# Performance work log

Measured on AMD Instinct MI355X. Metric: run time of the kernel, lower is better.

The kernel has to match this reference:

```python
import jax, jax.numpy as jnp
import numpy as np


def position_encoding(feature_size, d_model):
    pos = jnp.arange(feature_size, dtype=jnp.float32)[:, None]
    _2i = jnp.arange(0, d_model, 2, dtype=jnp.float32)
    ang = pos / jnp.power(10000.0, _2i / d_model)  # [F, D/2]
    pe = jnp.zeros((feature_size, d_model), dtype=jnp.float32)
    pe = pe.at[:, 0::2].set(jnp.sin(ang))
    pe = pe.at[:, 1::2].set(jnp.cos(ang))
    return pe


def setup_inputs() -> dict:
    key = jax.random.key(0)
    ks = jax.random.split(key, 11)
    B, F, D, T, V = 32, 512, 256, 32, 128
    sc = 0.02
    return {
        "f": jax.random.normal(ks[0], (B, F, D), dtype=jnp.float32),
        "decoder_input_ids": jax.random.randint(ks[1], (B, T), 0, V),
        "emb": sc * jax.random.normal(ks[2], (V, D), dtype=jnp.float32),
        "w_e": sc * jax.random.normal(ks[3], (D, D), dtype=jnp.float32),
        "w_h": sc * jax.random.normal(ks[4], (D, D), dtype=jnp.float32),
        "w_f": sc * jax.random.normal(ks[5], (D, D), dtype=jnp.float32),
        "w_q": sc * jax.random.normal(ks[6], (D, D), dtype=jnp.float32),
        "w_s": sc * jax.random.normal(ks[7], (D, D), dtype=jnp.float32),
        "w_g": sc * jax.random.normal(ks[8], (D, 2 * D), dtype=jnp.float32),
        "w_ih": sc * jax.random.normal(ks[9], (4 * D, 2 * D), dtype=jnp.float32),
        "w_hh": sc * jax.random.normal(ks[10], (4 * D, D), dtype=jnp.float32),
    }


def reference(f, decoder_input_ids, emb, w_e, w_h, w_f, w_q, w_s, w_g, w_ih, w_hh):
    B, F, D = f.shape
    q = position_encoding(F, D)                      # [F, D]
    dec = emb[decoder_input_ids]                     # [B, T, D]
    # loop-invariant attention terms, hoisted: w_f(f) + w_q(q)
    base = jnp.einsum('bfd,od->bfo', f, w_f) + (q @ w_q.T)[None]  # [B, F, D]
    fq = f + q[None]                                 # [B, F, D]

    def step(carry, x_t):
        h, cell, s, cp = carry
        # LSTMCell (bias=False), torch gate order i, f, g, o
        xin = jnp.concatenate([x_t, cp], axis=-1)    # [B, 2D]
        gates = xin @ w_ih.T + h @ w_hh.T            # [B, 4D]
        gi, gf, gg, go = jnp.split(gates, 4, axis=-1)
        cell = jax.nn.sigmoid(gf) * cell + jax.nn.sigmoid(gi) * jnp.tanh(gg)
        h = jax.nn.sigmoid(go) * jnp.tanh(cell)
        # Bahdanau-style energy; softmax over feature (last) dim per source
        t_in = jnp.tanh((h @ w_h.T)[:, None] + base + jnp.einsum('bfd,od->bfo', s, w_s))
        e = jnp.einsum('bfd,od->bfo', t_in, w_e)     # [B, F, D]
        alpha = jax.nn.softmax(e, axis=-1)
        s = s + alpha
        c = (alpha * f).sum(1)                       # [B, D]
        cp = (alpha * fq).sum(1)                     # [B, D]
        pred = jnp.concatenate([c, h], axis=-1) @ w_g.T  # [B, D]
        return (h, cell, s, cp), pred

    z = jnp.zeros((B, D), dtype=f.dtype)
    carry0 = (z, z, jnp.zeros_like(f), z)
    _, preds = jax.lax.scan(step, carry0, jnp.swapaxes(dec, 0, 1))  # [T, B, D]
    return jnp.swapaxes(preds, 0, 1)                 # [B, T, D]
```

## Files before the change

kernel.cpp:

```cpp
#include <hip/hip_runtime.h>
#include <math.h>

#define NB 32
#define NF 512
#define ND 256
#define NT 32
#define RPB 32
#define NTILE (NF / RPB)
#define NBLK (NB * NTILE)
#define XS 260

typedef __attribute__((ext_vector_type(8))) short bf16x8;
typedef __attribute__((ext_vector_type(4))) short bf16x4;
typedef __attribute__((ext_vector_type(4))) float f32x4;

__device__ __forceinline__ float sigmoidf_(float x) { return 1.0f / (1.0f + __expf(-x)); }

__device__ __forceinline__ short f2bf(float x) {
    union { float f; unsigned u; } v; v.f = x;
    unsigned r = (v.u + 0x7FFF + ((v.u >> 16) & 1)) >> 16;
    return (short)r;
}

#define AGENT __HIP_MEMORY_SCOPE_AGENT
__device__ __forceinline__ float AL(const float* p) {
    return __hip_atomic_load(p, __ATOMIC_RELAXED, AGENT);
}
__device__ __forceinline__ void AS(float* p, float v) {
    __hip_atomic_store(p, v, __ATOMIC_RELAXED, AGENT);
}
__device__ __forceinline__ int APOLL(int* p) {
    return __hip_atomic_fetch_add(p, 0, __ATOMIC_RELAXED, AGENT);
}
__device__ __forceinline__ void SIGNAL(int* p, int tid, int coop) {
    asm volatile("s_waitcnt vmcnt(0)" ::: "memory");
    __syncthreads();
    if (coop && tid == 0) __hip_atomic_fetch_add(p, 1, __ATOMIC_RELAXED, AGENT);
}
__device__ __forceinline__ void WAITGE(int* p, int tgt, int tid) {
    if (tid == 0) {
        while (APOLL(p) < tgt) __builtin_amdgcn_s_sleep(2);
    }
    __syncthreads();
}

__global__ void pe_kernel(float* __restrict__ q) {
    int p = blockIdx.x;
    int d = threadIdx.x;
    float i2 = (float)((d >> 1) << 1);
    float rate = expf(-9.210340371976184f * (i2 / (float)ND));
    float ang = (float)p * rate;
    q[p * ND + d] = (d & 1) ? cosf(ang) : sinf(ang);
}

__global__ void wcvt_kernel(const float* __restrict__ w, short* __restrict__ wb, int n) {
    int i = blockIdx.x * 256 + threadIdx.x;
    if (i < n) wb[i] = f2bf(w[i]);
}

__global__ void wprep_kernel(const float* __restrict__ w_ih, const float* __restrict__ w_hh,
                             const float* __restrict__ w_h, const float* __restrict__ w_g,
                             float* __restrict__ wcat, float* __restrict__ w_hT,
                             float* __restrict__ w_gT) {
    int j = blockIdx.x;
    int o = threadIdx.x;
    wcat[(size_t)j * 768 + o]       = w_ih[(size_t)j * 512 + o];
    wcat[(size_t)j * 768 + 256 + o] = w_ih[(size_t)j * 512 + 256 + o];
    wcat[(size_t)j * 768 + 512 + o] = w_hh[(size_t)j * 256 + o];
    if (j < ND)  w_hT[(size_t)j * ND + o] = w_h[(size_t)o * ND + j];
    if (j < 512) w_gT[(size_t)j * ND + o] = w_g[(size_t)o * 512 + j];
}

__global__ void qwq_kernel(const float* __restrict__ q, const float* __restrict__ w_q,
                           float* __restrict__ qwq) {
    int p = blockIdx.x;
    int o = threadIdx.x;
    __shared__ float qs[ND];
    qs[o] = q[(size_t)p * ND + o];
    __syncthreads();
    const float4* wr = (const float4*)(w_q + (size_t)o * ND);
    float acc = 0.f;
    for (int k4 = 0; k4 < ND / 4; ++k4) {
        float4 w = wr[k4];
        int k = 4 * k4;
        acc += qs[k] * w.x + qs[k + 1] * w.y + qs[k + 2] * w.z + qs[k + 3] * w.w;
    }
    qwq[(size_t)p * ND + o] = acc;
}

__global__ void base_kernel(const float* __restrict__ fin, const float* __restrict__ w_f,
                            const float* __restrict__ qwq, float* __restrict__ bsum) {
    int b = blockIdx.x / NTILE;
    int f0 = (blockIdx.x % NTILE) * RPB;
    int o = threadIdx.x;
    __shared__ float fs[RPB][ND];
    #pragma unroll
    for (int r = 0; r < RPB; ++r)
        fs[r][o] = fin[((size_t)(b * NF + f0 + r)) * ND + o];
    __syncthreads();
    float acc[RPB];
    #pragma unroll
    for (int r = 0; r < RPB; ++r) acc[r] = 0.f;
    const float4* wr = (const float4*)(w_f + (size_t)o * ND);
    for (int k4 = 0; k4 < ND / 4; ++k4) {
        float4 w = wr[k4];
        int k = 4 * k4;
        #pragma unroll
        for (int r = 0; r < RPB; ++r)
            acc[r] += fs[r][k] * w.x + fs[r][k + 1] * w.y + fs[r][k + 2] * w.z + fs[r][k + 3] * w.w;
    }
    #pragma unroll
    for (int r = 0; r < RPB; ++r)
        bsum[((size_t)(b * NF + f0 + r)) * ND + o] = acc[r] + qwq[(size_t)(f0 + r) * ND + o];
}

__global__ void __launch_bounds__(256, 2) dec_persist(
        int coop, int t0, int smask,
        const float* __restrict__ fin, const int* __restrict__ ids,
        const float* __restrict__ emb, const float* __restrict__ qpe,
        float* __restrict__ bsum,
        const float* __restrict__ wcat, const float* __restrict__ w_hT,
        const float* __restrict__ w_gT,
        const short* __restrict__ w_e_bf, const short* __restrict__ w_s_bf,
        float* __restrict__ h, float* __restrict__ cell,
        float* __restrict__ gatesT,
        float* __restrict__ cpart, float* __restrict__ cppart,
        int* __restrict__ acount, int* __restrict__ gcount, int* __restrict__ hflag,
        float* __restrict__ out) {
    int bid = blockIdx.x;
    int tid = threadIdx.x;
    int l = tid & 63;
    int wv = tid >> 6;
    int c15 = l & 15;
    int g = l >> 4;
    int c = l;
    int b = bid >> 4;
    int tile = bid & 15;
    int f0 = tile * RPB;
    int o0 = wv * 64;

    __shared__ __align__(16) short tin_bf[RPB * ND];
    __shared__ float xfer[RPB * XS];
    __shared__ float cred[2][1024];
    __shared__ float sred[RPB][5];
    char* tb = (char*)tin_bf;
    float* zl = xfer;
    float* zp = xfer;
    float* hn = xfer;
    float* hwhl = xfer + 256;

    const size_t CP = (size_t)NTILE * NB * ND;

    int tbeg = coop ? 0 : t0;
    int tend = coop ? NT : t0;

    for (int t = tbeg; t <= tend; ++t) {
        int prd = (t > 0) ? ((t - 1) & 1) : 0;

        if ((smask & 1) && t < NT) {
            if (coop) {
                if (tid == 0) {
                    while (APOLL(&acount[b]) < 16 * t) __builtin_amdgcn_s_sleep(2);
                    while (APOLL(&hflag[b]) < t) __builtin_amdgcn_s_sleep(2);
                }
                __syncthreads();
            }
            float xv = emb[(size_t)ids[b * NT + t] * ND + tid];
            float cpsum = 0.f;
            if (t > 0) {
                #pragma unroll
                for (int tl = 0; tl < NTILE; ++tl)
                    cpsum += AL(&cppart[prd * CP + ((size_t)tl * NB + b) * ND + tid]);
            }
            zl[tid] = xv;
            zl[256 + tid] = cpsum;
            zl[512 + tid] = AL(&h[(size_t)(t & 1) * NB * ND + b * ND + tid]);
            __syncthreads();
            int j0 = tile * 64 + wv * 16;
            for (int jj = 0; jj < 16; ++jj) {
                int j = j0 + jj;
                const float* wr = wcat + (size_t)j * 768;
                float s = 0.f;
                #pragma unroll
                for (int i = 0; i < 12; ++i)
                    s += wr[l + i * 64] * zl[l + i * 64];
                #pragma unroll
                for (int off = 1; off <= 32; off <<= 1)
                    s += __shfl_xor(s, off);
                if (l == 0) AS(&gatesT[(size_t)b * 1024 + j], s);
            }
            SIGNAL(&gcount[b], tid, coop);
        }

        if ((smask & 2) && t < NT && tile == 0) {
            if (coop) WAITGE(&gcount[b], 16 * (t + 1), tid);
            float gi = AL(&gatesT[(size_t)b * 1024 + tid]);
            float gf = AL(&gatesT[(size_t)b * 1024 + 256 + tid]);
            float gg = AL(&gatesT[(size_t)b * 1024 + 512 + tid]);
            float go = AL(&gatesT[(size_t)b * 1024 + 768 + tid]);
            float cold = cell[(size_t)b * ND + tid];
            float cnew = sigmoidf_(gf) * cold + sigmoidf_(gi) * tanhf(gg);
            float hval = sigmoidf_(go) * tanhf(cnew);
            cell[(size_t)b * ND + tid] = cnew;
            AS(&h[(size_t)((t + 1) & 1) * NB * ND + b * ND + tid], hval);
            SIGNAL(&hflag[b], tid, coop);
        }

        if ((smask & 2) && t > 0 && tile == 1) {
            if (coop && t == NT) {
                if (tid == 0) {
                    while (APOLL(&acount[b]) < 16 * t) __builtin_amdgcn_s_sleep(2);
                    while (APOLL(&hflag[b]) < t) __builtin_amdgcn_s_sleep(2);
                }
                __syncthreads();
            }
            float csum = 0.f;
            #pragma unroll
            for (int tl = 0; tl < NTILE; ++tl)
                csum += AL(&cpart[prd * CP + ((size_t)tl * NB + b) * ND + tid]);
            zp[tid] = csum;
            zp[256 + tid] = AL(&h[(size_t)(t & 1) * NB * ND + b * ND + tid]);
            __syncthreads();
            float p = 0.f;
            #pragma unroll 8
            for (int k = 0; k < 512; ++k)
                p += zp[k] * w_gT[(size_t)k * ND + tid];
            out[((size_t)b * NT + (t - 1)) * ND + tid] = p;
            __syncthreads();
        }

        if (t >= NT) continue;

        if (smask & 4) {
            if (coop) WAITGE(&hflag[b], t + 1, tid);
            hn[tid] = AL(&h[(size_t)((t + 1) & 1) * NB * ND + b * ND + tid]);
            __syncthreads();
            {
                float a = 0.f;
                #pragma unroll 8
                for (int k = 0; k < ND; ++k)
                    a += hn[k] * w_hT[(size_t)k * ND + tid];
                hwhl[tid] = a;
            }
            __syncthreads();

            float4 bsv4[8];
            {
                float4 hwh4 = *(const float4*)&hwhl[4 * c];
                #pragma unroll
                for (int i = 0; i < 8; ++i) {
                    int r = wv + 4 * i;
                    bsv4[i] = *(const float4*)(bsum + ((size_t)(b * NF + f0 + r)) * ND + 4 * c);
                    bf16x4 tv;
                    tv.x = f2bf(tanhf(hwh4.x + bsv4[i].x));
                    tv.y = f2bf(tanhf(hwh4.y + bsv4[i].y));
                    tv.z = f2bf(tanhf(hwh4.z + bsv4[i].z));
                    tv.w = f2bf(tanhf(hwh4.w + bsv4[i].w));
                    *(bf16x4*)(tb + ((r * 512 + 8 * c) ^ ((r & 7) << 4))) = tv;
                }
            }
            __syncthreads();

            f32x4 acc[2][4];
            #pragma unroll
            for (int mt = 0; mt < 2; ++mt)
                #pragma unroll
                for (int nt = 0; nt < 4; ++nt)
                    acc[mt][nt] = (f32x4)0.f;
            #pragma unroll
            for (int ks = 0; ks < 8; ++ks) {
                int kb = ks * 32 + g * 8;
                bf16x8 afr[2];
                #pragma unroll
                for (int mt = 0; mt < 2; ++mt) {
                    int row = mt * 16 + c15;
                    afr[mt] = *(const bf16x8*)(tb + ((row * 512 + kb * 2) ^ ((row & 7) << 4)));
                }
                #pragma unroll
                for (int nt = 0; nt < 4; ++nt) {
                    int o = o0 + nt * 16 + c15;
                    bf16x8 bfr = *(const bf16x8*)(w_e_bf + (size_t)o * ND + kb);
                    #pragma unroll
                    for (int mt = 0; mt < 2; ++mt)
                        acc[mt][nt] = __builtin_amdgcn_mfma_f32_16x16x32_bf16(afr[mt], bfr, acc[mt][nt], 0, 0, 0);
                }
            }

            {
                float ps[2][4];
                #pragma unroll
                for (int mt = 0; mt < 2; ++mt)
                    #pragma unroll
                    for (int reg = 0; reg < 4; ++reg) ps[mt][reg] = 0.f;
                #pragma unroll
                for (int mt = 0; mt < 2; ++mt)
                    #pragma unroll
                    for (int nt = 0; nt < 4; ++nt)
                        #pragma unroll
                        for (int reg = 0; reg < 4; ++reg) {
                            float a = __expf(acc[mt][nt][reg]);
                            acc[mt][nt][reg] = a;
                            ps[mt][reg] += a;
                        }
                #pragma unroll
                for (int off = 1; off <= 8; off <<= 1)
                    #pragma unroll
                    for (int mt = 0; mt < 2; ++mt)
                        #pragma unroll
                        for (int reg = 0; reg < 4; ++reg)
                            ps[mt][reg] += __shfl_xor(ps[mt][reg], off);
                if (c15 == 0) {
                    #pragma unroll
                    for (int mt = 0; mt < 2; ++mt)
                        #pragma unroll
                        for (int reg = 0; reg < 4; ++reg)
                            sred[mt * 16 + g * 4 + reg][wv] = ps[mt][reg];
                }
                __syncthreads();
                #pragma unroll
                for (int mt = 0; mt < 2; ++mt)
                    #pragma unroll
                    for (int reg = 0; reg < 4; ++reg) {
                        int r = mt * 16 + g * 4 + reg;
                        float inv = 1.0f / (sred[r][0] + sred[r][1] + sred[r][2] + sred[r][3]);
                        #pragma unroll
                        for (int nt = 0; nt < 4; ++nt)
                            acc[mt][nt][reg] *= inv;
                    }
            }

            #pragma unroll
            for (int mt = 0; mt < 2; ++mt)
                #pragma unroll
                for (int reg = 0; reg < 4; ++reg) {
                    int r = mt * 16 + g * 4 + reg;
                    #pragma unroll
                    for (int nt = 0; nt < 4; ++nt)
                        xfer[r * XS + o0 + nt * 16 + c15] = acc[mt][nt][reg];
                }
            __syncthreads();

            {
                float4 pc4 = {0.f, 0.f, 0.f, 0.f}, pcp4 = {0.f, 0.f, 0.f, 0.f};
                #pragma unroll
                for (int i = 0; i < 8; ++i) {
                    int r = wv + 4 * i;
                    float4 a4 = *(const float4*)&xfer[r * XS + 4 * c];
                    float4 f4 = *(const float4*)(fin + ((size_t)(b * NF + f0 + r)) * ND + 4 * c);
                    float4 q4 = *(const float4*)(qpe + ((size_t)(f0 + r)) * ND + 4 * c);
                    pc4.x += a4.x * f4.x;  pcp4.x += a4.x * (f4.x + q4.x);
                    pc4.y += a4.y * f4.y;  pcp4.y += a4.y * (f4.y + q4.y);
                    pc4.z += a4.z * f4.z;  pcp4.z += a4.z * (f4.z + q4.z);
                    pc4.w += a4.w * f4.w;  pcp4.w += a4.w * (f4.w + q4.w);
                    bf16x4 av;
                    av.x = f2bf(a4.x); av.y = f2bf(a4.y); av.z = f2bf(a4.z); av.w = f2bf(a4.w);
                    *(bf16x4*)(tb + ((r * 512 + 8 * c) ^ ((r & 7) << 4))) = av;
                }
                *(float4*)&cred[0][wv * 256 + 4 * c] = pc4;
                *(float4*)&cred[1][wv * 256 + 4 * c] = pcp4;
            }
            __syncthreads();

            {
                float pc  = cred[0][tid] + cred[0][256 + tid] + cred[0][512 + tid] + cred[0][768 + tid];
                float pcp = cred[1][tid] + cred[1][256 + tid] + cred[1][512 + tid] + cred[1][768 + tid];
                AS(&cpart [(size_t)(t & 1) * CP + ((size_t)tile * NB + b) * ND + tid], pc);
                AS(&cppart[(size_t)(t & 1) * CP + ((size_t)tile * NB + b) * ND + tid], pcp);
            }

            {
                f32x4 acc2[2][4];
                #pragma unroll
                for (int mt = 0; mt < 2; ++mt)
                    #pragma unroll
                    for (int nt = 0; nt < 4; ++nt)
                        acc2[mt][nt] = (f32x4)0.f;
                #pragma unroll
                for (int ks = 0; ks < 8; ++ks) {
                    int kb = ks * 32 + g * 8;
                    bf16x8 afr[2];
                    #pragma unroll
                    for (int mt = 0; mt < 2; ++mt) {
                        int row = mt * 16 + c15;
                        afr[mt] = *(const bf16x8*)(tb + ((row * 512 + kb * 2) ^ ((row & 7) << 4)));
                    }
                    #pragma unroll
                    for (int nt = 0; nt < 4; ++nt) {
                        int o = o0 + nt * 16 + c15;
                        bf16x8 bfr = *(const bf16x8*)(w_s_bf + (size_t)o * ND + kb);
                        #pragma unroll
                        for (int mt = 0; mt < 2; ++mt)
                            acc2[mt][nt] = __builtin_amdgcn_mfma_f32_16x16x32_bf16(afr[mt], bfr, acc2[mt][nt], 0, 0, 0);
                    }
                }
                __syncthreads();
                #pragma unroll
                for (int mt = 0; mt < 2; ++mt)
                    #pragma unroll
                    for (int reg = 0; reg < 4; ++reg) {
                        int r = mt * 16 + g * 4 + reg;
                        #pragma unroll
                        for (int nt = 0; nt < 4; ++nt)
                            xfer[r * XS + o0 + nt * 16 + c15] = acc2[mt][nt][reg];
                    }
            }
            __syncthreads();

            #pragma unroll
            for (int i = 0; i < 8; ++i) {
                int r = wv + 4 * i;
                float4 x4 = *(const float4*)&xfer[r * XS + 4 * c];
                float4 o4;
                o4.x = bsv4[i].x + x4.x;
                o4.y = bsv4[i].y + x4.y;
                o4.z = bsv4[i].z + x4.z;
                o4.w = bsv4[i].w + x4.w;
                *(float4*)(bsum + ((size_t)(b * NF + f0 + r)) * ND + 4 * c) = o4;
            }
            SIGNAL(&acount[b], tid, coop);
        }
    }
}

extern "C" void kernel_launch(void* const* d_in, const int* in_sizes, int n_in,
                              void* d_out, int out_size, void* d_ws, size_t ws_size,
                              hipStream_t stream) {
    const float* fin  = (const float*)d_in[0];
    const int*   ids  = (const int*)  d_in[1];
    const float* emb  = (const float*)d_in[2];
    const float* w_e  = (const float*)d_in[3];
    const float* w_h  = (const float*)d_in[4];
    const float* w_f  = (const float*)d_in[5];
    const float* w_q  = (const float*)d_in[6];
    const float* w_s  = (const float*)d_in[7];
    const float* w_g  = (const float*)d_in[8];
    const float* w_ih = (const float*)d_in[9];
    const float* w_hh = (const float*)d_in[10];
    float* out = (float*)d_out;
    float* ws  = (float*)d_ws;

    size_t off = 0;
    float* q      = ws + off; off += (size_t)NF * ND;
    float* qwq    = ws + off; off += (size_t)NF * ND;
    float* bsum   = ws + off; off += (size_t)NB * NF * ND;
    float* h      = ws + off; off += (size_t)2 * NB * ND;
    float* cell   = ws + off; off += (size_t)NB * ND;
    float* gatesT = ws + off; off += (size_t)NB * 1024;
    float* cpart  = ws + off; off += (size_t)2 * NTILE * NB * ND;
    float* cppart = ws + off; off += (size_t)2 * NTILE * NB * ND;
    float* wcat   = ws + off; off += (size_t)1024 * 768;
    float* w_hT   = ws + off; off += (size_t)ND * ND;
    float* w_gT   = ws + off; off += (size_t)512 * ND;
    short* w_e_bf = (short*)(ws + off); off += (size_t)ND * ND / 2;
    short* w_s_bf = (short*)(ws + off); off += (size_t)ND * ND / 2;
    int*   acount = (int*)(ws + off); off += 32;
    int*   gcount = (int*)(ws + off); off += 32;
    int*   hflag  = (int*)(ws + off); off += 32;

    hipMemsetAsync(h, 0, sizeof(float) * NB * ND, stream);
    hipMemsetAsync(cell, 0, sizeof(float) * NB * ND, stream);
    hipMemsetAsync(acount, 0, sizeof(int) * 96, stream);

    pe_kernel<<<NF, ND, 0, stream>>>(q);
    wcvt_kernel<<<ND * ND / 256, 256, 0, stream>>>(w_e, w_e_bf, ND * ND);
    wcvt_kernel<<<ND * ND / 256, 256, 0, stream>>>(w_s, w_s_bf, ND * ND);
    wprep_kernel<<<1024, ND, 0, stream>>>(w_ih, w_hh, w_h, w_g, wcat, w_hT, w_gT);
    qwq_kernel<<<NF, ND, 0, stream>>>(q, w_q, qwq);
    base_kernel<<<NB * NTILE, ND, 0, stream>>>(fin, w_f, qwq, bsum);

    int coop1 = 1, t00 = 0, smask7 = 7;
    void* args[] = {
        (void*)&coop1, (void*)&t00, (void*)&smask7,
        (void*)&fin, (void*)&ids, (void*)&emb, (void*)&q, (void*)&bsum,
        (void*)&wcat, (void*)&w_hT, (void*)&w_gT,
        (void*)&w_e_bf, (void*)&w_s_bf,
        (void*)&h, (void*)&cell, (void*)&gatesT,
        (void*)&cpart, (void*)&cppart,
        (void*)&acount, (void*)&gcount, (void*)&hflag,
        (void*)&out
    };
    hipError_t e = hipLaunchCooperativeKernel((void*)dec_persist, dim3(NBLK), dim3(ND),
                                              args, 0, stream);
    if (e != hipSuccess) {
        for (int t = 0; t <= NT; ++t) {
            if (t < NT)
                dec_persist<<<NBLK, ND, 0, stream>>>(0, t, 1, fin, ids, emb, q, bsum,
                        wcat, w_hT, w_gT, w_e_bf, w_s_bf, h, cell, gatesT,
                        cpart, cppart, acount, gcount, hflag, out);
            dec_persist<<<NBLK, ND, 0, stream>>>(0, t, 2, fin, ids, emb, q, bsum,
                    wcat, w_hT, w_gT, w_e_bf, w_s_bf, h, cell, gatesT,
                    cpart, cppart, acount, gcount, hflag, out);
            if (t < NT)
                dec_persist<<<NBLK, ND, 0, stream>>>(0, t, 4, fin, ids, emb, q, bsum,
                        wcat, w_hT, w_gT, w_e_bf, w_s_bf, h, cell, gatesT,
                        cpart, cppart, acount, gcount, hflag, out);
        }
    }
}
```

Before: 2.838 ms.

## Keep attention accumulator in registers and read features as bf16

```diff
diff --git a/kernel.cpp b/kernel.cpp
--- a/kernel.cpp
+++ b/kernel.cpp
@@ -20,6 +20,11 @@
     union { float f; unsigned u; } v; v.f = x;
     unsigned r = (v.u + 0x7FFF + ((v.u >> 16) & 1)) >> 16;
     return (short)r;
+}
+__device__ __forceinline__ float bf2f(short s) {
+    union { unsigned u; float f; } v;
+    v.u = ((unsigned)(unsigned short)s) << 16;
+    return v.f;
 }
 
 #define AGENT __HIP_MEMORY_SCOPE_AGENT
@@ -116,8 +121,8 @@
 
 __global__ void __launch_bounds__(256, 2) dec_persist(
         int coop, int t0, int smask,
-        const float* __restrict__ fin, const int* __restrict__ ids,
-        const float* __restrict__ emb, const float* __restrict__ qpe,
+        const short* __restrict__ fin_bf, const int* __restrict__ ids,
+        const float* __restrict__ emb, const short* __restrict__ q_bf,
         float* __restrict__ bsum,
         const float* __restrict__ wcat, const float* __restrict__ w_hT,
         const float* __restrict__ w_gT,
@@ -151,6 +156,15 @@
 
     const size_t CP = (size_t)NTILE * NB * ND;
 
+    float4 bsv4[8];
+    if (coop) {
+        #pragma unroll
+        for (int i = 0; i < 8; ++i) {
+            int r = wv + 4 * i;
+            bsv4[i] = *(const float4*)(bsum + ((size_t)(b * NF + f0 + r)) * ND + 4 * c);
+        }
+    }
+
     int tbeg = coop ? 0 : t0;
     int tend = coop ? NT : t0;
 
@@ -244,13 +258,13 @@
             }
             __syncthreads();
 
-            float4 bsv4[8];
             {
                 float4 hwh4 = *(const float4*)&hwhl[4 * c];
                 #pragma unroll
                 for (int i = 0; i < 8; ++i) {
                     int r = wv + 4 * i;
-                    bsv4[i] = *(const float4*)(bsum + ((size_t)(b * NF + f0 + r)) * ND + 4 * c);
+                    if (!coop)
+                        bsv4[i] = *(const float4*)(bsum + ((size_t)(b * NF + f0 + r)) * ND + 4 * c);
                     bf16x4 tv;
                     tv.x = f2bf(tanhf(hwh4.x + bsv4[i].x));
                     tv.y = f2bf(tanhf(hwh4.y + bsv4[i].y));
@@ -346,12 +360,14 @@
                 for (int i = 0; i < 8; ++i) {
                     int r = wv + 4 * i;
                     float4 a4 = *(const float4*)&xfer[r * XS + 4 * c];
-                    float4 f4 = *(const float4*)(fin + ((size_t)(b * NF + f0 + r)) * ND + 4 * c);
-                    float4 q4 = *(const float4*)(qpe + ((size_t)(f0 + r)) * ND + 4 * c);
-                    pc4.x += a4.x * f4.x;  pcp4.x += a4.x * (f4.x + q4.x);
-                    pc4.y += a4.y * f4.y;  pcp4.y += a4.y * (f4.y + q4.y);
-                    pc4.z += a4.z * f4.z;  pcp4.z += a4.z * (f4.z + q4.z);
-                    pc4.w += a4.w * f4.w;  pcp4.w += a4.w * (f4.w + q4.w);
+                    bf16x4 f4b = *(const bf16x4*)(fin_bf + ((size_t)(b * NF + f0 + r)) * ND + 4 * c);
+                    bf16x4 q4b = *(const bf16x4*)(q_bf + ((size_t)(f0 + r)) * ND + 4 * c);
+                    float fx = bf2f(f4b.x), fy = bf2f(f4b.y), fz = bf2f(f4b.z), fw = bf2f(f4b.w);
+                    float qx = bf2f(q4b.x), qy = bf2f(q4b.y), qz = bf2f(q4b.z), qw = bf2f(q4b.w);
+                    pc4.x += a4.x * fx;  pcp4.x += a4.x * (fx + qx);
+                    pc4.y += a4.y * fy;  pcp4.y += a4.y * (fy + qy);
+                    pc4.z += a4.z * fz;  pcp4.z += a4.z * (fz + qz);
+                    pc4.w += a4.w * fw;  pcp4.w += a4.w * (fw + qw);
                     bf16x4 av;
                     av.x = f2bf(a4.x); av.y = f2bf(a4.y); av.z = f2bf(a4.z); av.w = f2bf(a4.w);
                     *(bf16x4*)(tb + ((r * 512 + 8 * c) ^ ((r & 7) << 4))) = av;
@@ -410,12 +426,12 @@
             for (int i = 0; i < 8; ++i) {
                 int r = wv + 4 * i;
                 float4 x4 = *(const float4*)&xfer[r * XS + 4 * c];
-                float4 o4;
-                o4.x = bsv4[i].x + x4.x;
-                o4.y = bsv4[i].y + x4.y;
-                o4.z = bsv4[i].z + x4.z;
-                o4.w = bsv4[i].w + x4.w;
-                *(float4*)(bsum + ((size_t)(b * NF + f0 + r)) * ND + 4 * c) = o4;
+                bsv4[i].x += x4.x;
+                bsv4[i].y += x4.y;
+                bsv4[i].z += x4.z;
+                bsv4[i].w += x4.w;
+                if (!coop)
+                    *(float4*)(bsum + ((size_t)(b * NF + f0 + r)) * ND + 4 * c) = bsv4[i];
             }
             SIGNAL(&acount[b], tid, coop);
         }
@@ -453,6 +469,8 @@
     float* w_gT   = ws + off; off += (size_t)512 * ND;
     short* w_e_bf = (short*)(ws + off); off += (size_t)ND * ND / 2;
     short* w_s_bf = (short*)(ws + off); off += (size_t)ND * ND / 2;
+    short* fin_bf = (short*)(ws + off); off += (size_t)NB * NF * ND / 2;
+    short* q_bf   = (short*)(ws + off); off += (size_t)NF * ND / 2;
     int*   acount = (int*)(ws + off); off += 32;
     int*   gcount = (int*)(ws + off); off += 32;
     int*   hflag  = (int*)(ws + off); off += 32;
@@ -464,6 +482,8 @@
     pe_kernel<<<NF, ND, 0, stream>>>(q);
     wcvt_kernel<<<ND * ND / 256, 256, 0, stream>>>(w_e, w_e_bf, ND * ND);
     wcvt_kernel<<<ND * ND / 256, 256, 0, stream>>>(w_s, w_s_bf, ND * ND);
+    wcvt_kernel<<<NB * NF * ND / 256, 256, 0, stream>>>(fin, fin_bf, NB * NF * ND);
+    wcvt_kernel<<<NF * ND / 256, 256, 0, stream>>>(q, q_bf, NF * ND);
     wprep_kernel<<<1024, ND, 0, stream>>>(w_ih, w_hh, w_h, w_g, wcat, w_hT, w_gT);
     qwq_kernel<<<NF, ND, 0, stream>>>(q, w_q, qwq);
     base_kernel<<<NB * NTILE, ND, 0, stream>>>(fin, w_f, qwq, bsum);
@@ -471,7 +491,7 @@
     int coop1 = 1, t00 = 0, smask7 = 7;
     void* args[] = {
         (void*)&coop1, (void*)&t00, (void*)&smask7,
-        (void*)&fin, (void*)&ids, (void*)&emb, (void*)&q, (void*)&bsum,
+        (void*)&fin_bf, (void*)&ids, (void*)&emb, (void*)&q_bf, (void*)&bsum,
         (void*)&wcat, (void*)&w_hT, (void*)&w_gT,
         (void*)&w_e_bf, (void*)&w_s_bf,
         (void*)&h, (void*)&cell, (void*)&gatesT,
@@ -484,14 +504,14 @@
     if (e != hipSuccess) {
         for (int t = 0; t <= NT; ++t) {
             if (t < NT)
-                dec_persist<<<NBLK, ND, 0, stream>>>(0, t, 1, fin, ids, emb, q, bsum,
+                dec_persist<<<NBLK, ND, 0, stream>>>(0, t, 1, fin_bf, ids, emb, q_bf, bsum,
                         wcat, w_hT, w_gT, w_e_bf, w_s_bf, h, cell, gatesT,
                         cpart, cppart, acount, gcount, hflag, out);
-            dec_persist<<<NBLK, ND, 0, stream>>>(0, t, 2, fin, ids, emb, q, bsum,
+            dec_persist<<<NBLK, ND, 0, stream>>>(0, t, 2, fin_bf, ids, emb, q_bf, bsum,
                     wcat, w_hT, w_gT, w_e_bf, w_s_bf, h, cell, gatesT,
                     cpart, cppart, acount, gcount, hflag, out);
             if (t < NT)
-                dec_persist<<<NBLK, ND, 0, stream>>>(0, t, 4, fin, ids, emb, q, bsum,
+                dec_persist<<<NBLK, ND, 0, stream>>>(0, t, 4, fin_bf, ids, emb, q_bf, bsum,
                         wcat, w_hT, w_gT, w_e_bf, w_s_bf, h, cell, gatesT,
                         cpart, cppart, acount, gcount, hflag, out);
         }
```

After: 2.763 ms. 2.6% less time.
